# Optimization experiments

Hardware: AMD Instinct MI355X
Metric: run time of the kernel (lower is better)

## Reference

```python
import jax, jax.numpy as jnp
import numpy as np

B, N, D, PS = 8, 64, 64, 4          # batch, patches, per-patch dim, pooling size (N must equal D)
C_IN, LTF, LTI, LTO = 512, 512, 512, 512
L = D // PS


def setup_inputs() -> dict:
    key = jax.random.key(0)
    ks = jax.random.split(key, 7)
    s = 0.02
    return {
        "x": jax.random.normal(ks[0], (B, N * D, C_IN), dtype=jnp.float32),
        "W_in": jax.random.normal(ks[1], (C_IN, 3 * LTF), dtype=jnp.float32) * s,
        "b_in": jax.random.normal(ks[2], (3 * LTF,), dtype=jnp.float32) * s,
        "W_inter": jax.random.normal(ks[3], (LTF, LTI), dtype=jnp.float32) * s,
        "b_inter": jax.random.normal(ks[4], (LTI,), dtype=jnp.float32) * s,
        "W_last": jax.random.normal(ks[5], (LTI, LTO), dtype=jnp.float32) * s,
        "b_last": jax.random.normal(ks[6], (LTO,), dtype=jnp.float32) * s,
    }


def _lin(t, W, b):
    # channel-wise Linear on [B, C, N, d] maps (permute->Linear->permute fused into one einsum)
    return jnp.einsum('bcnd,ck->bknd', t, W) + b[None, :, None, None]


def reference(x, W_in, b_in, W_inter, b_inter, W_last, b_last):
    # seq2spatial: [B, N*d, C] -> [B, C, N, d]
    xs = jnp.transpose(x.reshape(B, N, D, C_IN), (0, 3, 1, 2))

    qkv = _lin(xs, W_in, b_in)                       # [B, 3*ltf, N, d]
    Q, K, V = jnp.split(qkv, 3, axis=1)              # each [B, ltf, N, d]

    def pool(t):  # avg_pool1d over N with kernel=stride=PS
        return t.reshape(B, t.shape[1], N // PS, PS, D).mean(axis=3)

    q = pool(Q)                                      # [B, ltf, L, d]
    k = pool(K)                                      # [B, ltf, L, d]

    def inter_last(t):
        # latent_inter_: Linear + softmax over channel dim; latent_last_: Linear (identity act)
        t = jax.nn.softmax(_lin(t, W_inter, b_inter), axis=1)
        return _lin(t, W_last, b_last)

    Qk = inter_last(jnp.einsum('bcnd,bcld->bcnl', Q, k))   # [B, lto, N, L]
    qK = inter_last(jnp.einsum('bcld,bcnd->bcln', q, K))   # [B, lto, L, N]
    Vp = inter_last(V)                                     # [B, lto, N, d]

    qKV = jnp.einsum('bcln,bcnd->bcld', qK, Vp)            # [B, lto, L, d]
    return jnp.einsum('bcnl,bcld->bcnd', Qk, qKV)          # [B, lto, N, d]
```

## Files before the change

### kernel.cpp

```cpp
#include <hip/hip_runtime.h>

typedef unsigned short u16;
typedef __attribute__((ext_vector_type(8))) short s16x8;
typedef __attribute__((ext_vector_type(4))) short s16x4;
typedef __attribute__((ext_vector_type(4))) float f32x4;

__device__ __forceinline__ u16 f2bf(float f){
  union { float f; unsigned u; } v; v.f = f;
  unsigned r = v.u + 0x7FFFu + ((v.u >> 16) & 1u);
  return (u16)(r >> 16);
}
__device__ __forceinline__ float bf2f(u16 h){
  union { unsigned u; float f; } v; v.u = ((unsigned)h) << 16;
  return v.f;
}
__device__ __forceinline__ f32x4 mfma16(s16x8 a, s16x8 b, f32x4 c){
  return __builtin_amdgcn_mfma_f32_16x16x32_bf16(a, b, c, 0, 0, 0);
}
__device__ __forceinline__ void gload16(const void* g, void* l){
  __builtin_amdgcn_global_load_lds((const __attribute__((address_space(1))) void*)g,
                                   (__attribute__((address_space(3))) void*)l, 16, 0, 0);
}
__device__ __forceinline__ int flidx(int k, int c){
  return ((k >> 4) * 16 + (c >> 5)) * 512 + ((c >> 3) & 3) * 128 + (k & 15) * 8 + (c & 7);
}

__global__ __launch_bounds__(256) void k0prep(
    const float* __restrict__ W_in, const float* __restrict__ W_inter, const float* __restrict__ W_last,
    u16* __restrict__ WT_in, u16* __restrict__ WTi_rm, u16* __restrict__ WiFL, u16* __restrict__ WlFL,
    const float* __restrict__ x, u16* __restrict__ xb)
{
  if (blockIdx.x < 2048){
    const int t = blockIdx.x * 256 + threadIdx.x;
    if (t < 1024 * 512){ const int k = t >> 9, c = t & 511; WT_in[t] = f2bf(W_in[c * 1536 + k]); }
    if (t < 512 * 512){
      const int k = t >> 9, c = t & 511;
      const int fl = flidx(k, c);
      const u16 wi = f2bf(W_inter[c * 512 + k]);
      WTi_rm[t] = wi;
      WiFL[fl]  = wi;
      WlFL[fl]  = f2bf(W_last[c * 512 + k]);
    }
  } else {
    const int t = (blockIdx.x - 2048) * 256 + threadIdx.x;
    const f32x4* src = (const f32x4*)x + (size_t)t * 2;
    f32x4 a = src[0], b = src[1];
    alignas(16) u16 h[8];
    #pragma unroll
    for (int i = 0; i < 4; ++i){ h[i] = f2bf(a[i]); h[4 + i] = f2bf(b[i]); }
    *(s16x8*)&xb[(size_t)t * 8] = *(const s16x8*)h;
  }
}

__global__ __launch_bounds__(256) void k0b_wvi(
    const float* __restrict__ W_in, const float* __restrict__ W_inter,
    const u16* __restrict__ WTi_rm, const float* __restrict__ b_in, const float* __restrict__ b_inter,
    u16* __restrict__ WviFL, float* __restrict__ b_vi)
{
  __shared__ u16 A_lds[64][72];
  if (blockIdx.x >= 16){
    float* r = (float*)&A_lds[0][0];
    const int k = (blockIdx.x - 16) * 64 + (threadIdx.x & 63);
    const int pt = threadIdx.x >> 6;
    float s = 0.f;
    #pragma unroll 4
    for (int c = pt * 128; c < pt * 128 + 128; ++c)
      s += b_in[1024 + c] * W_inter[c * 512 + k];
    r[pt * 64 + (threadIdx.x & 63)] = s;
    __syncthreads();
    if (pt == 0){
      const int kk = threadIdx.x;
      b_vi[k] = b_inter[k] + r[kk] + r[64 + kk] + r[128 + kk] + r[192 + kk];
    }
    return;
  }
  const int kt = blockIdx.x & 1;
  const int m0 = (blockIdx.x >> 1) * 64;
  const int tid = threadIdx.x;
  const int w = tid >> 6, l = tid & 63;
  const int l15 = l & 15, lg = l >> 4;
  const int kbase = kt * 256 + w * 64;
  f32x4 acc[4][4] = {};
  const int sr = tid >> 2, sc = (tid & 3) * 16;
  for (int c0 = 0; c0 < 512; c0 += 64){
    __syncthreads();
    {
      const f32x4* src = (const f32x4*)(W_in + (size_t)(m0 + sr) * 1536 + 1024 + c0 + sc);
      f32x4 a0 = src[0], a1 = src[1], a2 = src[2], a3 = src[3];
      alignas(16) u16 h[16];
      #pragma unroll
      for (int i = 0; i < 4; ++i){ h[i] = f2bf(a0[i]); h[4+i] = f2bf(a1[i]); h[8+i] = f2bf(a2[i]); h[12+i] = f2bf(a3[i]); }
      *(s16x8*)&A_lds[sr][sc]     = *(const s16x8*)&h[0];
      *(s16x8*)&A_lds[sr][sc + 8] = *(const s16x8*)&h[8];
    }
    __syncthreads();
    #pragma unroll
    for (int kk = 0; kk < 2; ++kk){
      s16x8 af[4];
      #pragma unroll
      for (int m = 0; m < 4; ++m)
        af[m] = *(const s16x8*)&A_lds[m * 16 + l15][kk * 32 + lg * 8];
      #pragma unroll
      for (int kc = 0; kc < 4; ++kc){
        s16x8 bf = *(const s16x8*)&WTi_rm[(size_t)(kbase + kc * 16 + l15) * 512 + c0 + kk * 32 + lg * 8];
        #pragma unroll
        for (int m = 0; m < 4; ++m) acc[m][kc] = mfma16(af[m], bf, acc[m][kc]);
      }
    }
  }
  #pragma unroll
  for (int kc = 0; kc < 4; ++kc){
    const int k = kbase + kc * 16 + l15;
    #pragma unroll
    for (int m = 0; m < 4; ++m){
      const int cin = m0 + m * 16 + lg * 4;
      uint2 pk;
      pk.x = (unsigned)f2bf(acc[m][kc][0]) | ((unsigned)f2bf(acc[m][kc][1]) << 16);
      pk.y = (unsigned)f2bf(acc[m][kc][2]) | ((unsigned)f2bf(acc[m][kc][3]) << 16);
      *(uint2*)&WviFL[flidx(k, cin)] = pk;
    }
  }
}

__global__ __launch_bounds__(256) void k1_qk(
    const u16* __restrict__ xb, const u16* __restrict__ WT_in, const float* __restrict__ b_in,
    u16* __restrict__ Qp, u16* __restrict__ Kp)
{
  __shared__ __align__(16) u16 As[128 * 64];
  __shared__ __align__(16) u16 Bs[128 * 64];
  const int t = threadIdx.x;
  const int w = t >> 6, l = t & 63;
  const int l15 = l & 15, lg = l >> 4;
  const int wr = w >> 1, wc = w & 1;
  const size_t Mbase = (size_t)blockIdx.y * 128;
  const int Nbase = blockIdx.x * 128;

  f32x4 acc[4][4] = {};
  for (int c0 = 0; c0 < 512; c0 += 64){
    __syncthreads();
    #pragma unroll
    for (int it = 0; it < 4; ++it){
      const int g = it * 256 + t;
      const int row = g >> 3, cc = g & 7;
      const int sc = (cc ^ (row & 7)) * 8;
      gload16(&xb[(Mbase + row) * 512 + c0 + sc], &As[g * 8]);
    }
    #pragma unroll
    for (int it = 0; it < 4; ++it){
      const int g = it * 256 + t;
      const int row = g >> 3, cc = g & 7;
      const int sc = (cc ^ (row & 7)) * 8;
      gload16(&WT_in[(size_t)(Nbase + row) * 512 + c0 + sc], &Bs[g * 8]);
    }
    __syncthreads();
    #pragma unroll
    for (int kk = 0; kk < 2; ++kk){
      s16x8 af[4], bf[4];
      #pragma unroll
      for (int m = 0; m < 4; ++m){
        const int row = wr * 64 + m * 16 + l15;
        af[m] = *(const s16x8*)&As[row * 64 + ((kk * 4 + lg) ^ (row & 7)) * 8];
      }
      #pragma unroll
      for (int n = 0; n < 4; ++n){
        const int row = wc * 64 + n * 16 + l15;
        bf[n] = *(const s16x8*)&Bs[row * 64 + ((kk * 4 + lg) ^ (row & 7)) * 8];
      }
      #pragma unroll
      for (int n = 0; n < 4; ++n)
        #pragma unroll
        for (int m = 0; m < 4; ++m) acc[m][n] = mfma16(af[m], bf[n], acc[m][n]);
    }
  }
  const int b = (int)(Mbase >> 12);
  const int ploc = ((int)Mbase & 4095) + wr * 64;
  #pragma unroll
  for (int n = 0; n < 4; ++n){
    const int kglob = Nbase + wc * 64 + n * 16 + l15;
    const float bias = b_in[kglob];
    u16* dst = (kglob < 512) ? Qp : Kp;
    const int kq = kglob & 511;
    #pragma unroll
    for (int m = 0; m < 4; ++m){
      const int p = ploc + m * 16 + lg * 4;
      uint2 pk;
      pk.x = (unsigned)f2bf(acc[m][n][0] + bias) | ((unsigned)f2bf(acc[m][n][1] + bias) << 16);
      pk.y = (unsigned)f2bf(acc[m][n][2] + bias) | ((unsigned)f2bf(acc[m][n][3] + bias) << 16);
      *(uint2*)&dst[((size_t)b * 512 + kq) * 4096 + p] = pk;
    }
  }
}

__global__ __launch_bounds__(512) void k3_scores(
    const u16* __restrict__ Qp, const u16* __restrict__ Kp, u16* __restrict__ T12)
{
  __shared__ __align__(16) u16 buf[1024 * 20];
  const bool s2 = blockIdx.x >= 256;
  const int blk = blockIdx.x & 255;
  const int b = blk >> 5, c0 = (blk & 31) * 16;
  const int w = threadIdx.x >> 6;
  const int l = threadIdx.x & 63, l15 = l & 15, lg = l >> 4;
  #pragma unroll
  for (int half = 0; half < 2; ++half){
    const int c = c0 + half * 8 + w;
    const int ci = half * 8 + w;
    const u16* Qr = Qp + ((size_t)b * 512 + c) * 4096;
    const u16* Kr = Kp + ((size_t)b * 512 + c) * 4096;
    if (!s2){
      f32x4 acc[4] = {};
      #pragma unroll
      for (int kk = 0; kk < 2; ++kk){
        float pv[8] = {};
        #pragma unroll
        for (int r = 0; r < 4; ++r){
          s16x8 v = *(const s16x8*)&Kr[(4 * l15 + r) * 64 + kk * 32 + lg * 8];
          #pragma unroll
          for (int j = 0; j < 8; ++j) pv[j] += bf2f((u16)v[j]);
        }
        alignas(16) u16 bh[8];
        #pragma unroll
        for (int j = 0; j < 8; ++j) bh[j] = f2bf(pv[j] * 0.25f);
        s16x8 bf = *(const s16x8*)bh;
        #pragma unroll
        for (int m = 0; m < 4; ++m){
          s16x8 af = *(const s16x8*)&Qr[(m * 16 + l15) * 64 + kk * 32 + lg * 8];
          acc[m] = mfma16(af, bf, acc[m]);
        }
      }
      #pragma unroll
      for (int m = 0; m < 4; ++m)
        #pragma unroll
        for (int j = 0; j < 4; ++j)
          buf[((m * 16 + lg * 4 + j) * 16 + l15) * 20 + ci] = f2bf(acc[m][j]);
    } else {
      f32x4 acc[4] = {};
      #pragma unroll
      for (int kk = 0; kk < 2; ++kk){
        float pv[8] = {};
        #pragma unroll
        for (int r = 0; r < 4; ++r){
          s16x8 v = *(const s16x8*)&Qr[(4 * l15 + r) * 64 + kk * 32 + lg * 8];
          #pragma unroll
          for (int j = 0; j < 8; ++j) pv[j] += bf2f((u16)v[j]);
        }
        alignas(16) u16 ah[8];
        #pragma unroll
        for (int j = 0; j < 8; ++j) ah[j] = f2bf(pv[j] * 0.25f);
        s16x8 af = *(const s16x8*)ah;
        #pragma unroll
        for (int nt = 0; nt < 4; ++nt){
          s16x8 bf = *(const s16x8*)&Kr[(nt * 16 + l15) * 64 + kk * 32 + lg * 8];
          acc[nt] = mfma16(af, bf, acc[nt]);
        }
      }
      #pragma unroll
      for (int nt = 0; nt < 4; ++nt)
        #pragma unroll
        for (int j = 0; j < 4; ++j)
          buf[((lg * 4 + j) * 64 + nt * 16 + l15) * 20 + ci] = f2bf(acc[nt][j]);
    }
  }
  __syncthreads();
  const int off = s2 ? 1024 : 0;
  for (int rr = (int)threadIdx.x; rr < 1024; rr += 512){
    uint2 a  = *(const uint2*)&buf[rr * 20 + 0];
    uint2 bq = *(const uint2*)&buf[rr * 20 + 4];
    uint2 cq = *(const uint2*)&buf[rr * 20 + 8];
    uint2 dq = *(const uint2*)&buf[rr * 20 + 12];
    u16* dst = &T12[((size_t)b * 2048 + off + rr) * 512 + c0];
    *(uint4*)&dst[0] = make_uint4(a.x, a.y, bq.x, bq.y);
    *(uint4*)&dst[8] = make_uint4(cq.x, cq.y, dq.x, dq.y);
  }
}

__global__ __launch_bounds__(512) void k4_interlast(
    const u16* __restrict__ TV, const u16* __restrict__ Tab,
    u16* __restrict__ OV, u16* __restrict__ Oab,
    const u16* __restrict__ WviFL, const float* __restrict__ b_vi,
    const u16* __restrict__ WiFL, const float* __restrict__ b_ab,
    const u16* __restrict__ WlFL, const float* __restrict__ bl)
{
  __shared__ __align__(16) u16 smem[64 * 512];
  __shared__ __align__(16) float red2[64 * 8];
  const bool isV = blockIdx.x < 64;
  const int bx = isV ? (int)blockIdx.x : (int)blockIdx.x - 64;
  const int Pn = isV ? 4096 : 2048;
  const u16* T = isV ? TV : Tab;
  u16* O = isV ? OV : Oab;
  const u16* W1 = isV ? WviFL : WiFL;
  const float* bi = isV ? b_vi : b_ab;
  const int b = blockIdx.y;
  const int p0 = bx * 64;
  const int w = threadIdx.x >> 6, l = threadIdx.x & 63;
  const int l15 = l & 15, lg = l >> 4;
  const u16* Tb = T + (size_t)b * Pn * 512;

  #pragma unroll
  for (int it = 0; it < 8; ++it){
    const int g = it * 512 + threadIdx.x;
    const int row = g >> 6, cc = g & 63;
    const int sc = ((cc & 7) ^ (row & 7)) | (cc & 56);
    gload16(&Tb[(size_t)(p0 + row) * 512 + sc * 8], &smem[g * 8]);
  }
  __syncthreads();

  f32x4 acc[4][4] = {};
  {
    s16x8 bfn[4];
    #pragma unroll
    for (int kc = 0; kc < 4; ++kc)
      bfn[kc] = *(const s16x8*)&W1[(size_t)(((w * 4 + kc) * 16) * 64 + l) * 8];
    for (int cs = 0; cs < 16; ++cs){
      s16x8 bfc[4];
      #pragma unroll
      for (int kc = 0; kc < 4; ++kc) bfc[kc] = bfn[kc];
      if (cs < 15){
        #pragma unroll
        for (int kc = 0; kc < 4; ++kc)
          bfn[kc] = *(const s16x8*)&W1[(size_t)(((w * 4 + kc) * 16 + cs + 1) * 64 + l) * 8];
      }
      s16x8 af[4];
      #pragma unroll
      for (int pr = 0; pr < 4; ++pr){
        const int row = pr * 16 + l15;
        const int gi = cs * 4 + lg;
        const int gs = ((gi & 7) ^ (row & 7)) | (gi & 56);
        af[pr] = *(const s16x8*)&smem[row * 512 + gs * 8];
      }
      #pragma unroll
      for (int kc = 0; kc < 4; ++kc)
        #pragma unroll
        for (int pr = 0; pr < 4; ++pr) acc[pr][kc] = mfma16(af[pr], bfc[kc], acc[pr][kc]);
    }
  }
  __syncthreads();

  #pragma unroll
  for (int kc = 0; kc < 4; ++kc){
    const float bias = bi[w * 64 + kc * 16 + l15];
    #pragma unroll
    for (int pr = 0; pr < 4; ++pr)
      #pragma unroll
      for (int j = 0; j < 4; ++j)
        acc[pr][kc][j] = __expf(acc[pr][kc][j] + bias);
  }
  #pragma unroll
  for (int pr = 0; pr < 4; ++pr)
    #pragma unroll
    for (int j = 0; j < 4; ++j){
      float s = (acc[pr][0][j] + acc[pr][1][j]) + (acc[pr][2][j] + acc[pr][3][j]);
      s += __shfl_xor(s, 1); s += __shfl_xor(s, 2);
      s += __shfl_xor(s, 4); s += __shfl_xor(s, 8);
      if (l15 == 0) red2[(pr * 16 + lg * 4 + j) * 8 + w] = s;
    }
  #pragma unroll
  for (int pr = 0; pr < 4; ++pr)
    #pragma unroll
    for (int j = 0; j < 4; ++j){
      const int row = pr * 16 + lg * 4 + j;
      const int sw = (row & 7) << 3;
      #pragma unroll
      for (int kc = 0; kc < 4; ++kc)
        smem[row * 512 + ((w * 64 + kc * 16 + l15) ^ sw)] = f2bf(acc[pr][kc][j]);
    }
  __syncthreads();

  float inv[4][4];
  {
    const f32x4* r = (const f32x4*)&red2[l * 8];
    f32x4 r0 = r[0], r1 = r[1];
    float S = ((r0[0] + r0[1]) + (r0[2] + r0[3])) + ((r1[0] + r1[1]) + (r1[2] + r1[3]));
    #pragma unroll
    for (int pr = 0; pr < 4; ++pr)
      #pragma unroll
      for (int j = 0; j < 4; ++j)
        inv[pr][j] = 1.f / __shfl(S, pr * 16 + lg * 4 + j);
  }
  f32x4 z[4][4] = {};
  {
    const int swr = (l15 & 7) << 3;
    s16x8 bfn[4];
    #pragma unroll
    for (int kc = 0; kc < 4; ++kc)
      bfn[kc] = *(const s16x8*)&WlFL[(size_t)(((w * 4 + kc) * 16) * 64 + l) * 8];
    for (int ks = 0; ks < 16; ++ks){
      s16x8 bfc[4];
      #pragma unroll
      for (int kc = 0; kc < 4; ++kc) bfc[kc] = bfn[kc];
      if (ks < 15){
        #pragma unroll
        for (int kc = 0; kc < 4; ++kc)
          bfn[kc] = *(const s16x8*)&WlFL[(size_t)(((w * 4 + kc) * 16 + ks + 1) * 64 + l) * 8];
      }
      const int k0 = ks * 32 + lg * 8;
      s16x8 af[4];
      #pragma unroll
      for (int pr = 0; pr < 4; ++pr)
        af[pr] = *(const s16x8*)&smem[(pr * 16 + l15) * 512 + (k0 ^ swr)];
      #pragma unroll
      for (int kc = 0; kc < 4; ++kc)
        #pragma unroll
        for (int pr = 0; pr < 4; ++pr) z[pr][kc] = mfma16(af[pr], bfc[kc], z[pr][kc]);
    }
  }
  u16* Ob = O + (size_t)b * 512 * Pn;
  #pragma unroll
  for (int kc = 0; kc < 4; ++kc){
    const int k2 = w * 64 + kc * 16 + l15;
    const float bias = bl[k2];
    #pragma unroll
    for (int pr = 0; pr < 4; ++pr){
      uint2 pk;
      pk.x = (unsigned)f2bf(z[pr][kc][0] * inv[pr][0] + bias) | ((unsigned)f2bf(z[pr][kc][1] * inv[pr][1] + bias) << 16);
      pk.y = (unsigned)f2bf(z[pr][kc][2] * inv[pr][2] + bias) | ((unsigned)f2bf(z[pr][kc][3] * inv[pr][3] + bias) << 16);
      *(uint2*)&Ob[(size_t)k2 * Pn + p0 + pr * 16 + lg * 4] = pk;
    }
  }
}

__global__ __launch_bounds__(256) void k56(
    const u16* __restrict__ O12, const u16* __restrict__ Vp, float* __restrict__ out)
{
  __shared__ __align__(16) u16 Vt[4][64 * 68];
  __shared__ __align__(16) u16 Tt[4][16 * 64];
  const int w = threadIdx.x >> 6;
  const int W = blockIdx.x * 4 + w;
  const int b = W >> 9, c = W & 511;
  const int l = threadIdx.x & 63, l15 = l & 15, lg = l >> 4;
  const u16* base = O12 + ((size_t)b * 512 + c) * 2048;
  const u16* Qr = base;
  const u16* qr = base + 1024;
  const u16* vr = Vp + ((size_t)b * 512 + c) * 4096;
  u16* vt = &Vt[w][0];
  u16* tt = &Tt[w][0];
  {
    const s16x8* src = (const s16x8*)&vr[l * 64];
    #pragma unroll
    for (int i = 0; i < 8; ++i){
      s16x8 v = src[i];
      *(s16x4*)&vt[l * 68 + i * 8]     = __builtin_shufflevector(v, v, 0, 1, 2, 3);
      *(s16x4*)&vt[l * 68 + i * 8 + 4] = __builtin_shufflevector(v, v, 4, 5, 6, 7);
    }
  }
  f32x4 acc1[4] = {};
  #pragma unroll
  for (int kk = 0; kk < 2; ++kk){
    s16x8 af = *(const s16x8*)&qr[l15 * 64 + kk * 32 + lg * 8];
    #pragma unroll
    for (int dt = 0; dt < 4; ++dt){
      alignas(16) u16 bh[8];
      #pragma unroll
      for (int j = 0; j < 8; ++j)
        bh[j] = vt[(kk * 32 + lg * 8 + j) * 68 + dt * 16 + l15];
      acc1[dt] = mfma16(af, *(const s16x8*)bh, acc1[dt]);
    }
  }
  #pragma unroll
  for (int dt = 0; dt < 4; ++dt)
    #pragma unroll
    for (int j = 0; j < 4; ++j)
      tt[(lg * 4 + j) * 64 + dt * 16 + l15] = f2bf(acc1[dt][j]);
  s16x8 af2[4] = {};
  if (lg < 2){
    #pragma unroll
    for (int m = 0; m < 4; ++m)
      af2[m] = *(const s16x8*)&Qr[(m * 16 + l15) * 16 + lg * 8];
  }
  f32x4 acc2[4][4] = {};
  #pragma unroll
  for (int dt = 0; dt < 4; ++dt){
    alignas(16) u16 bh[8] = {};
    if (lg < 2){
      #pragma unroll
      for (int j = 0; j < 8; ++j)
        bh[j] = tt[(lg * 8 + j) * 64 + dt * 16 + l15];
    }
    s16x8 bf = *(const s16x8*)bh;
    #pragma unroll
    for (int m = 0; m < 4; ++m) acc2[m][dt] = mfma16(af2[m], bf, acc2[m][dt]);
  }
  float* ob = out + ((size_t)b * 512 + c) * 4096;
  #pragma unroll
  for (int m = 0; m < 4; ++m)
    #pragma unroll
    for (int dt = 0; dt < 4; ++dt)
      #pragma unroll
      for (int j = 0; j < 4; ++j)
        ob[(m * 16 + lg * 4 + j) * 64 + dt * 16 + l15] = acc2[m][dt][j];
}

extern "C" void kernel_launch(void* const* d_in, const int* in_sizes, int n_in,
                              void* d_out, int out_size, void* d_ws, size_t ws_size,
                              hipStream_t stream)
{
  (void)in_sizes; (void)n_in; (void)out_size; (void)ws_size;
  const float* x       = (const float*)d_in[0];
  const float* W_in    = (const float*)d_in[1];
  const float* b_in    = (const float*)d_in[2];
  const float* W_inter = (const float*)d_in[3];
  const float* b_inter = (const float*)d_in[4];
  const float* W_last  = (const float*)d_in[5];
  const float* b_last  = (const float*)d_in[6];
  float* out = (float*)d_out;

  char* ws = (char*)d_ws;
  size_t off = 0;
  auto alloc = [&](size_t bytes) -> u16* {
    u16* p = (u16*)(ws + off);
    off += (bytes + 255) & ~(size_t)255;
    return p;
  };
  u16*  WT_in  = alloc((size_t)1024 * 512 * 2);
  u16*  WTi_rm = alloc((size_t)512 * 512 * 2);
  u16*  WiFL   = alloc((size_t)512 * 512 * 2);
  u16*  WlFL   = alloc((size_t)512 * 512 * 2);
  u16*  WviFL  = alloc((size_t)512 * 512 * 2);
  float* b_vi  = (float*)alloc((size_t)512 * 4);
  u16*  xb     = alloc((size_t)8 * 4096 * 512 * 2);
  u16*  Qp     = alloc((size_t)8 * 512 * 4096 * 2);
  u16*  Kp     = alloc((size_t)8 * 512 * 4096 * 2);
  u16*  T12    = alloc((size_t)8 * 2048 * 512 * 2);
  u16*  Vpp    = Qp;
  u16*  O12    = Kp;

  k0prep<<<10240, 256, 0, stream>>>(W_in, W_inter, W_last, WT_in, WTi_rm, WiFL, WlFL, x, xb);
  k0b_wvi<<<24, 256, 0, stream>>>(W_in, W_inter, WTi_rm, b_in, b_inter, WviFL, b_vi);
  k1_qk<<<dim3(8, 256), 256, 0, stream>>>(xb, WT_in, b_in, Qp, Kp);
  k3_scores<<<512, 512, 0, stream>>>(Qp, Kp, T12);
  k4_interlast<<<dim3(96, 8), 512, 0, stream>>>(xb, T12, Vpp, O12,
                                                WviFL, b_vi, WiFL, b_inter, WlFL, b_last);
  k56<<<1024, 256, 0, stream>>>(O12, Vpp, out);
}
```

Measured before the change: 353.4 us.

## Halve interlast row tile, fold log2e into weights, vectorize k56 LDS transpose

The inter/last kernel now handles 32 rows per block instead of 64. That doubles the grid, halves LDS use and accumulator registers, and the weight fragments become a two-stage ring with the cs loop fully unrolled. The softmax exponent is changed to exp2 by pre-scaling W_inter and the biases by log2(e) in the prep kernels, and a separate scaled bias buffer is added. In k56 the intermediate tile is stored transposed with padding, so the B-fragment becomes a single 16-byte LDS load instead of eight scalar reads. The trade-off is that each block re-reads the weight matrices for fewer rows, which doubles weight traffic per output row.

Measured after the change: 400.5 us. 13.3% more time.

```diff
diff --git a/kernel.cpp b/kernel.cpp
--- a/kernel.cpp
+++ b/kernel.cpp
@@ -4,6 +4,8 @@
 typedef __attribute__((ext_vector_type(8))) short s16x8;
 typedef __attribute__((ext_vector_type(4))) short s16x4;
 typedef __attribute__((ext_vector_type(4))) float f32x4;
+
+#define LOG2E 1.4426950408889634f
 
 __device__ __forceinline__ u16 f2bf(float f){
   union { float f; unsigned u; } v; v.f = f;
@@ -36,7 +38,7 @@
     if (t < 512 * 512){
       const int k = t >> 9, c = t & 511;
       const int fl = flidx(k, c);
-      const u16 wi = f2bf(W_inter[c * 512 + k]);
+      const u16 wi = f2bf(W_inter[c * 512 + k] * LOG2E);
       WTi_rm[t] = wi;
       WiFL[fl]  = wi;
       WlFL[fl]  = f2bf(W_last[c * 512 + k]);
@@ -55,7 +57,7 @@
 __global__ __launch_bounds__(256) void k0b_wvi(
     const float* __restrict__ W_in, const float* __restrict__ W_inter,
     const u16* __restrict__ WTi_rm, const float* __restrict__ b_in, const float* __restrict__ b_inter,
-    u16* __restrict__ WviFL, float* __restrict__ b_vi)
+    u16* __restrict__ WviFL, float* __restrict__ b_vi, float* __restrict__ b_abs)
 {
   __shared__ u16 A_lds[64][72];
   if (blockIdx.x >= 16){
@@ -70,7 +72,8 @@
     __syncthreads();
     if (pt == 0){
       const int kk = threadIdx.x;
-      b_vi[k] = b_inter[k] + r[kk] + r[64 + kk] + r[128 + kk] + r[192 + kk];
+      b_vi[k]  = (b_inter[k] + r[kk] + r[64 + kk] + r[128 + kk] + r[192 + kk]) * LOG2E;
+      b_abs[k] = b_inter[k] * LOG2E;
     }
     return;
   }
@@ -277,26 +280,26 @@
     const u16* __restrict__ TV, const u16* __restrict__ Tab,
     u16* __restrict__ OV, u16* __restrict__ Oab,
     const u16* __restrict__ WviFL, const float* __restrict__ b_vi,
-    const u16* __restrict__ WiFL, const float* __restrict__ b_ab,
+    const u16* __restrict__ WiFL, const float* __restrict__ b_abs,
     const u16* __restrict__ WlFL, const float* __restrict__ bl)
 {
-  __shared__ __align__(16) u16 smem[64 * 512];
-  __shared__ __align__(16) float red2[64 * 8];
-  const bool isV = blockIdx.x < 64;
-  const int bx = isV ? (int)blockIdx.x : (int)blockIdx.x - 64;
+  __shared__ __align__(16) u16 smem[32 * 512];
+  __shared__ __align__(16) float red2[32 * 8];
+  const bool isV = blockIdx.x < 128;
+  const int bx = isV ? (int)blockIdx.x : (int)blockIdx.x - 128;
   const int Pn = isV ? 4096 : 2048;
   const u16* T = isV ? TV : Tab;
   u16* O = isV ? OV : Oab;
   const u16* W1 = isV ? WviFL : WiFL;
-  const float* bi = isV ? b_vi : b_ab;
+  const float* bi = isV ? b_vi : b_abs;
   const int b = blockIdx.y;
-  const int p0 = bx * 64;
+  const int p0 = bx * 32;
   const int w = threadIdx.x >> 6, l = threadIdx.x & 63;
   const int l15 = l & 15, lg = l >> 4;
   const u16* Tb = T + (size_t)b * Pn * 512;
 
   #pragma unroll
-  for (int it = 0; it < 8; ++it){
+  for (int it = 0; it < 4; ++it){
     const int g = it * 512 + threadIdx.x;
     const int row = g >> 6, cc = g & 63;
     const int sc = ((cc & 7) ^ (row & 7)) | (cc & 56);
@@ -304,24 +307,19 @@
   }
   __syncthreads();
 
-  f32x4 acc[4][4] = {};
+  f32x4 acc[2][4] = {};
   {
-    s16x8 bfn[4];
-    #pragma unroll
-    for (int kc = 0; kc < 4; ++kc)
-      bfn[kc] = *(const s16x8*)&W1[(size_t)(((w * 4 + kc) * 16) * 64 + l) * 8];
+    s16x8 bf[2][4];
+    #pragma unroll
+    for (int kc = 0; kc < 4; ++kc){
+      bf[0][kc] = *(const s16x8*)&W1[(size_t)(((w * 4 + kc) * 16 + 0) * 64 + l) * 8];
+      bf[1][kc] = *(const s16x8*)&W1[(size_t)(((w * 4 + kc) * 16 + 1) * 64 + l) * 8];
+    }
+    #pragma unroll
     for (int cs = 0; cs < 16; ++cs){
-      s16x8 bfc[4];
-      #pragma unroll
-      for (int kc = 0; kc < 4; ++kc) bfc[kc] = bfn[kc];
-      if (cs < 15){
-        #pragma unroll
-        for (int kc = 0; kc < 4; ++kc)
-          bfn[kc] = *(const s16x8*)&W1[(size_t)(((w * 4 + kc) * 16 + cs + 1) * 64 + l) * 8];
-      }
-      s16x8 af[4];
-      #pragma unroll
-      for (int pr = 0; pr < 4; ++pr){
+      s16x8 af[2];
+      #pragma unroll
+      for (int pr = 0; pr < 2; ++pr){
         const int row = pr * 16 + l15;
         const int gi = cs * 4 + lg;
         const int gs = ((gi & 7) ^ (row & 7)) | (gi & 56);
@@ -330,7 +328,12 @@
       #pragma unroll
       for (int kc = 0; kc < 4; ++kc)
         #pragma unroll
-        for (int pr = 0; pr < 4; ++pr) acc[pr][kc] = mfma16(af[pr], bfc[kc], acc[pr][kc]);
+        for (int pr = 0; pr < 2; ++pr) acc[pr][kc] = mfma16(af[pr], bf[cs & 1][kc], acc[pr][kc]);
+      if (cs < 14){
+        #pragma unroll
+        for (int kc = 0; kc < 4; ++kc)
+          bf[cs & 1][kc] = *(const s16x8*)&W1[(size_t)(((w * 4 + kc) * 16 + cs + 2) * 64 + l) * 8];
+      }
     }
   }
   __syncthreads();
@@ -339,13 +342,13 @@
   for (int kc = 0; kc < 4; ++kc){
     const float bias = bi[w * 64 + kc * 16 + l15];
     #pragma unroll
-    for (int pr = 0; pr < 4; ++pr)
+    for (int pr = 0; pr < 2; ++pr)
       #pragma unroll
       for (int j = 0; j < 4; ++j)
-        acc[pr][kc][j] = __expf(acc[pr][kc][j] + bias);
-  }
-  #pragma unroll
-  for (int pr = 0; pr < 4; ++pr)
+        acc[pr][kc][j] = __builtin_amdgcn_exp2f(acc[pr][kc][j] + bias);
+  }
+  #pragma unroll
+  for (int pr = 0; pr < 2; ++pr)
     #pragma unroll
     for (int j = 0; j < 4; ++j){
       float s = (acc[pr][0][j] + acc[pr][1][j]) + (acc[pr][2][j] + acc[pr][3][j]);
@@ -354,53 +357,53 @@
       if (l15 == 0) red2[(pr * 16 + lg * 4 + j) * 8 + w] = s;
     }
   #pragma unroll
-  for (int pr = 0; pr < 4; ++pr)
+  for (int pr = 0; pr < 2; ++pr)
     #pragma unroll
     for (int j = 0; j < 4; ++j){
       const int row = pr * 16 + lg * 4 + j;
-      const int sw = (row & 7) << 3;
+      const int sw = ((row & 7) << 3) ^ ((row & 8) << 1);
       #pragma unroll
       for (int kc = 0; kc < 4; ++kc)
         smem[row * 512 + ((w * 64 + kc * 16 + l15) ^ sw)] = f2bf(acc[pr][kc][j]);
     }
   __syncthreads();
 
-  float inv[4][4];
+  float inv[2][4];
   {
-    const f32x4* r = (const f32x4*)&red2[l * 8];
+    const f32x4* r = (const f32x4*)&red2[(l & 31) * 8];
     f32x4 r0 = r[0], r1 = r[1];
     float S = ((r0[0] + r0[1]) + (r0[2] + r0[3])) + ((r1[0] + r1[1]) + (r1[2] + r1[3]));
     #pragma unroll
-    for (int pr = 0; pr < 4; ++pr)
+    for (int pr = 0; pr < 2; ++pr)
       #pragma unroll
       for (int j = 0; j < 4; ++j)
         inv[pr][j] = 1.f / __shfl(S, pr * 16 + lg * 4 + j);
   }
-  f32x4 z[4][4] = {};
+  f32x4 z[2][4] = {};
   {
-    const int swr = (l15 & 7) << 3;
-    s16x8 bfn[4];
-    #pragma unroll
-    for (int kc = 0; kc < 4; ++kc)
-      bfn[kc] = *(const s16x8*)&WlFL[(size_t)(((w * 4 + kc) * 16) * 64 + l) * 8];
+    const int swr = ((l15 & 7) << 3) ^ ((l15 & 8) << 1);
+    s16x8 bf[2][4];
+    #pragma unroll
+    for (int kc = 0; kc < 4; ++kc){
+      bf[0][kc] = *(const s16x8*)&WlFL[(size_t)(((w * 4 + kc) * 16 + 0) * 64 + l) * 8];
+      bf[1][kc] = *(const s16x8*)&WlFL[(size_t)(((w * 4 + kc) * 16 + 1) * 64 + l) * 8];
+    }
+    #pragma unroll
     for (int ks = 0; ks < 16; ++ks){
-      s16x8 bfc[4];
-      #pragma unroll
-      for (int kc = 0; kc < 4; ++kc) bfc[kc] = bfn[kc];
-      if (ks < 15){
+      const int k0 = ks * 32 + lg * 8;
+      s16x8 af[2];
+      #pragma unroll
+      for (int pr = 0; pr < 2; ++pr)
+        af[pr] = *(const s16x8*)&smem[(pr * 16 + l15) * 512 + (k0 ^ swr)];
+      #pragma unroll
+      for (int kc = 0; kc < 4; ++kc)
+        #pragma unroll
+        for (int pr = 0; pr < 2; ++pr) z[pr][kc] = mfma16(af[pr], bf[ks & 1][kc], z[pr][kc]);
+      if (ks < 14){
         #pragma unroll
         for (int kc = 0; kc < 4; ++kc)
-          bfn[kc] = *(const s16x8*)&WlFL[(size_t)(((w * 4 + kc) * 16 + ks + 1) * 64 + l) * 8];
-      }
-      const int k0 = ks * 32 + lg * 8;
-      s16x8 af[4];
-      #pragma unroll
-      for (int pr = 0; pr < 4; ++pr)
-        af[pr] = *(const s16x8*)&smem[(pr * 16 + l15) * 512 + (k0 ^ swr)];
-      #pragma unroll
-      for (int kc = 0; kc < 4; ++kc)
-        #pragma unroll
-        for (int pr = 0; pr < 4; ++pr) z[pr][kc] = mfma16(af[pr], bfc[kc], z[pr][kc]);
+          bf[ks & 1][kc] = *(const s16x8*)&WlFL[(size_t)(((w * 4 + kc) * 16 + ks + 2) * 64 + l) * 8];
+      }
     }
   }
   u16* Ob = O + (size_t)b * 512 * Pn;
@@ -409,7 +412,7 @@
     const int k2 = w * 64 + kc * 16 + l15;
     const float bias = bl[k2];
     #pragma unroll
-    for (int pr = 0; pr < 4; ++pr){
+    for (int pr = 0; pr < 2; ++pr){
       uint2 pk;
       pk.x = (unsigned)f2bf(z[pr][kc][0] * inv[pr][0] + bias) | ((unsigned)f2bf(z[pr][kc][1] * inv[pr][1] + bias) << 16);
       pk.y = (unsigned)f2bf(z[pr][kc][2] * inv[pr][2] + bias) | ((unsigned)f2bf(z[pr][kc][3] * inv[pr][3] + bias) << 16);
@@ -422,7 +425,7 @@
     const u16* __restrict__ O12, const u16* __restrict__ Vp, float* __restrict__ out)
 {
   __shared__ __align__(16) u16 Vt[4][64 * 68];
-  __shared__ __align__(16) u16 Tt[4][16 * 64];
+  __shared__ __align__(16) u16 Tt[4][64 * 24];
   const int w = threadIdx.x >> 6;
   const int W = blockIdx.x * 4 + w;
   const int b = W >> 9, c = W & 511;
@@ -456,10 +459,12 @@
     }
   }
   #pragma unroll
-  for (int dt = 0; dt < 4; ++dt)
-    #pragma unroll
-    for (int j = 0; j < 4; ++j)
-      tt[(lg * 4 + j) * 64 + dt * 16 + l15] = f2bf(acc1[dt][j]);
+  for (int dt = 0; dt < 4; ++dt){
+    alignas(8) u16 hj[4];
+    #pragma unroll
+    for (int j = 0; j < 4; ++j) hj[j] = f2bf(acc1[dt][j]);
+    *(s16x4*)&tt[(dt * 16 + l15) * 24 + lg * 4] = *(const s16x4*)hj;
+  }
   s16x8 af2[4] = {};
   if (lg < 2){
     #pragma unroll
@@ -469,13 +474,9 @@
   f32x4 acc2[4][4] = {};
   #pragma unroll
   for (int dt = 0; dt < 4; ++dt){
-    alignas(16) u16 bh[8] = {};
-    if (lg < 2){
-      #pragma unroll
-      for (int j = 0; j < 8; ++j)
-        bh[j] = tt[(lg * 8 + j) * 64 + dt * 16 + l15];
-    }
-    s16x8 bf = *(const s16x8*)bh;
+    s16x8 bf = {};
+    if (lg < 2)
+      bf = *(const s16x8*)&tt[(dt * 16 + l15) * 24 + lg * 8];
     #pragma unroll
     for (int m = 0; m < 4; ++m) acc2[m][dt] = mfma16(af2[m], bf, acc2[m][dt]);
   }
@@ -516,6 +517,7 @@
   u16*  WlFL   = alloc((size_t)512 * 512 * 2);
   u16*  WviFL  = alloc((size_t)512 * 512 * 2);
   float* b_vi  = (float*)alloc((size_t)512 * 4);
+  float* b_abs = (float*)alloc((size_t)512 * 4);
   u16*  xb     = alloc((size_t)8 * 4096 * 512 * 2);
   u16*  Qp     = alloc((size_t)8 * 512 * 4096 * 2);
   u16*  Kp     = alloc((size_t)8 * 512 * 4096 * 2);
@@ -524,10 +526,10 @@
   u16*  O12    = Kp;
 
   k0prep<<<10240, 256, 0, stream>>>(W_in, W_inter, W_last, WT_in, WTi_rm, WiFL, WlFL, x, xb);
-  k0b_wvi<<<24, 256, 0, stream>>>(W_in, W_inter, WTi_rm, b_in, b_inter, WviFL, b_vi);
+  k0b_wvi<<<24, 256, 0, stream>>>(W_in, W_inter, WTi_rm, b_in, b_inter, WviFL, b_vi, b_abs);
   k1_qk<<<dim3(8, 256), 256, 0, stream>>>(xb, WT_in, b_in, Qp, Kp);
   k3_scores<<<512, 512, 0, stream>>>(Qp, Kp, T12);
-  k4_interlast<<<dim3(96, 8), 512, 0, stream>>>(xb, T12, Vpp, O12,
-                                                WviFL, b_vi, WiFL, b_inter, WlFL, b_last);
+  k4_interlast<<<dim3(192, 8), 512, 0, stream>>>(xb, T12, Vpp, O12,
+                                                 WviFL, b_vi, WiFL, b_abs, WlFL, b_last);
   k56<<<1024, 256, 0, stream>>>(O12, Vpp, out);
 }
```
